# Kernel tuning notes

Hardware: AMD Instinct MI355X
Metric: run time of the kernel (lower is better)

Reference implementation:

```python
import math
import jax, jax.numpy as jnp
from jax import lax
import numpy as np

B, CIN, COUT, K, SD, NCLS, H, W = 8, 512, 512, 3, 512, 35, 64, 64
EPS_DEMOD = 1e-8
EPS_IN = 1e-5  # torch InstanceNorm2d default eps


def _equal_linear(x, w, b):
    # EqualLinear: F.linear(x, w * (1/sqrt(in_dim))) + b  (lr_mul=1)
    return x @ (w.T * (1.0 / math.sqrt(w.shape[1]))) + b


def setup_inputs() -> dict:
    key = jax.random.key(0)
    ks = jax.random.split(key, 8)
    return {
        "input": jax.random.normal(ks[0], (B, CIN, H, W), jnp.float32),
        "style": jax.random.normal(ks[1], (B, SD), jnp.float32),
        "class_style": jax.random.normal(ks[2], (NCLS, SD), jnp.float32),
        "weight": jax.random.normal(ks[3], (1, COUT, CIN, K, K), jnp.float32),
        "mod_w": jax.random.normal(ks[4], (CIN, SD), jnp.float32),
        "mod_b": jnp.ones((CIN,), jnp.float32),  # bias_init=1
        "cw_w": jax.random.normal(ks[5], (COUT, SD), jnp.float32),
        "cw_b": jnp.ones((COUT,), jnp.float32),
        "cb_w": jax.random.normal(ks[6], (COUT, SD), jnp.float32),
        "cb_b": jnp.ones((COUT,), jnp.float32),
        "label_class_dict": jax.random.randint(ks[7], (B, H, W), 0, NCLS),
    }


def reference(input, style, class_style, weight, mod_w, mod_b, cw_w, cw_b, cb_w, cb_b, label_class_dict):
    scale = 1.0 / math.sqrt(CIN * K * K)
    pad = K // 2

    # per-sample style modulation of weights
    s = _equal_linear(style, mod_w, mod_b)                 # [B, CIN]
    w = scale * weight * s[:, None, :, None, None]         # [B, COUT, CIN, K, K]
    demod = lax.rsqrt(jnp.sum(w * w, axis=(2, 3, 4)) + EPS_DEMOD)  # [B, COUT]
    w = w * demod[:, :, None, None, None]

    # grouped conv (groups = batch) == vmap of per-sample conv
    def conv_one(x, wb):  # x [CIN,H,W], wb [COUT,CIN,K,K]
        return lax.conv_general_dilated(
            x[None], wb, window_strides=(1, 1), padding=[(pad, pad), (pad, pad)],
            dimension_numbers=("NCHW", "OIHW", "NCHW"))[0]

    out = jax.vmap(conv_one)(input, w)                     # [B, COUT, H, W]

    # param-free instance norm (biased variance, no affine)
    mu = out.mean(axis=(2, 3), keepdims=True)
    var = out.var(axis=(2, 3), keepdims=True)
    out = (out - mu) * lax.rsqrt(var + EPS_IN)

    # CLADE per-class affine from class_style, gathered via label map
    cw = _equal_linear(class_style, cw_w, cw_b)            # [NCLS, COUT]
    cb = _equal_linear(class_style, cb_w, cb_b)            # [NCLS, COUT]
    class_weight = jnp.transpose(cw[label_class_dict], (0, 3, 1, 2))  # [B,COUT,H,W]
    class_bias = jnp.transpose(cb[label_class_dict], (0, 3, 1, 2))
    return out * class_weight + class_bias
```

## Files before the change

kernel.cpp:

```cpp
#include <hip/hip_runtime.h>

typedef unsigned short u16;
typedef unsigned int u32;
typedef __attribute__((ext_vector_type(8))) short short8;
typedef __attribute__((ext_vector_type(4))) float floatx4;

__device__ inline float bf2f(u16 h) {
  union { u32 u; float f; } v; v.u = ((u32)h) << 16; return v.f;
}
__device__ inline u16 f2bf(float f) {
  union { float f; u32 u; } v; v.f = f;
  u32 u = v.u;
  return (u16)((u + 0x7fffu + ((u >> 16) & 1u)) >> 16);
}
__device__ inline float ldf(const void* p, int i, int isbf) {
  return isbf ? bf2f(((const u16*)p)[i]) : ((const float*)p)[i];
}

__global__ void sniff_kernel(const u32* __restrict__ w, int* __restrict__ flag) {
  __shared__ int cnt;
  if (threadIdx.x == 0) cnt = 0;
  __syncthreads();
  int c = 0;
  #pragma unroll
  for (int i = 0; i < 4; ++i) {
    u32 v = w[1024 + threadIdx.x * 4 + i];
    int e = (v >> 7) & 0xFF;
    if (e >= 96 && e <= 160) c++;
  }
  atomicAdd(&cnt, c);
  __syncthreads();
  if (threadIdx.x == 0) *flag = (cnt >= 154) ? 1 : 0;
}

__global__ void styles_kernel(const void* __restrict__ style, const void* __restrict__ class_style,
                              const void* __restrict__ mod_w, const void* __restrict__ mod_b,
                              const void* __restrict__ cw_w, const void* __restrict__ cw_b,
                              const void* __restrict__ cb_w, const void* __restrict__ cb_b,
                              const int* __restrict__ flagp,
                              float* __restrict__ s, float* __restrict__ cw, float* __restrict__ cb) {
  const int isbf = *flagp;
  int row = blockIdx.x;
  const void *vec, *wm, *bias; float* out; int voff;
  if (row < 8)        { vec = style;       voff = row*512;        wm = mod_w; bias = mod_b; out = s  + row*512; }
  else if (row < 43)  { vec = class_style; voff = (row-8)*512;    wm = cw_w;  bias = cw_b;  out = cw + (row-8)*512; }
  else                { vec = class_style; voff = (row-43)*512;   wm = cb_w;  bias = cb_b;  out = cb + (row-43)*512; }
  __shared__ float v[512];
  for (int i = threadIdx.x; i < 512; i += 256) v[i] = ldf(vec, voff + i, isbf);
  __syncthreads();
  const float inv = 0.04419417382415922f;
  for (int o = threadIdx.x; o < 512; o += 256) {
    float acc = 0.f;
    if (isbf) {
      for (int k = 0; k < 512; ++k) acc += bf2f(((const u16*)wm)[o*512 + k]) * v[k];
    } else {
      const float4* wr = (const float4*)((const float*)wm + o*512);
      for (int k = 0; k < 128; ++k) {
        float4 p = wr[k];
        acc += p.x*v[k*4+0] + p.y*v[k*4+1] + p.z*v[k*4+2] + p.w*v[k*4+3];
      }
    }
    out[o] = acc * inv + ldf(bias, o, isbf);
  }
}

__global__ void wprep_kernel(const void* __restrict__ weight, const int* __restrict__ flagp,
                             u16* __restrict__ wT, float* __restrict__ wsqT) {
  const int isbf = *flagp;
  const int co = blockIdx.x;
  __shared__ float wsmem[4608];
  for (int i = threadIdx.x; i < 4608; i += 256)
    wsmem[i] = ldf(weight, co*4608 + i, isbf);
  __syncthreads();
  for (int ci = threadIdx.x; ci < 512; ci += 256) {
    float sq = 0.f;
    const int ck = ci >> 5, cin = ci & 31;
    #pragma unroll
    for (int tap = 0; tap < 9; ++tap) {
      float fv = wsmem[ci*9 + tap];
      sq += fv*fv;
      wT[(size_t)(((ck*9 + tap)*512) + co)*32 + cin] = f2bf(fv);
    }
    wsqT[ci*512 + co] = sq;
  }
}

__global__ void xtrans_kernel(const void* __restrict__ x, const float* __restrict__ s,
                              const int* __restrict__ flagp, u16* __restrict__ xT) {
  const int isbf = *flagp;
  const int t = threadIdx.x;
  const int w = t & 63, cq = t >> 6;
  const int b = blockIdx.z, h = blockIdx.y;
  const int ck = blockIdx.x;
  const int ci0 = ck*32 + cq*8;
  float f[8];
  #pragma unroll
  for (int j = 0; j < 8; ++j) {
    float xv = ldf(x, (((b*512) + ci0 + j)*64 + h)*64 + w, isbf);
    f[j] = xv * s[b*512 + ci0 + j];
  }
  u32 outp[4];
  #pragma unroll
  for (int i = 0; i < 4; ++i)
    outp[i] = (u32)f2bf(f[2*i]) | ((u32)f2bf(f[2*i+1]) << 16);
  uint4 po = {outp[0], outp[1], outp[2], outp[3]};
  *(uint4*)&xT[(size_t)((((b*16 + ck)*64 + h)*64 + w)*32) + cq*8] = po;
}

__global__ __launch_bounds__(256, 2) void conv_kernel(const u16* __restrict__ xT, const u16* __restrict__ wT,
                                                      float* __restrict__ y, float* __restrict__ part) {
  __shared__ __align__(16) u16 xs[4*10*66*8];
  __shared__ __align__(16) u16 wsm[9*4*64*8];
  const int tid = threadIdx.x;
  const int lane = tid & 63;
  const int wid = tid >> 6;
  const int hb = blockIdx.x, b = blockIdx.y;
  const int ct0 = blockIdx.z * 64;
  const int h0 = hb * 8;

  if (tid < 80) {
    int q = tid / 20, rem = tid % 20, dr = rem >> 1, side = rem & 1;
    uint4 z = {0,0,0,0};
    *(uint4*)&xs[(((q*10 + dr)*66) + side*65)*8] = z;
  }

  floatx4 acc[4][8];
  #pragma unroll
  for (int i = 0; i < 4; ++i) {
    #pragma unroll
    for (int j = 0; j < 8; ++j) acc[i][j] = (floatx4)(0.f);
  }

  const int m = lane & 15, qd = lane >> 4;

  for (int ck = 0; ck < 16; ++ck) {
    __syncthreads();

    #pragma unroll
    for (int j = 0; j < 10; ++j) {
      int g = tid + j*256;
      int q = g & 3, c64 = (g >> 2) & 63, dr = g >> 8;
      int hin = h0 + dr - 1;
      uint4 v = {0,0,0,0};
      if (hin >= 0 && hin <= 63)
        v = *(const uint4*)&xT[(size_t)((((b*16 + ck)*64 + hin)*64 + c64)*32) + q*8];
      *(uint4*)&xs[(((q*10 + dr)*66) + 1 + c64)*8] = v;
    }
    #pragma unroll
    for (int j = 0; j < 9; ++j) {
      int g = tid + j*256;
      int q = g & 3, co = (g >> 2) & 63, tap = g >> 8;
      uint4 v = *(const uint4*)&wT[(size_t)(((ck*9 + tap)*512) + ct0 + co)*32 + q*8];
      *(uint4*)&wsm[(((tap*4 + q)*64) + (co ^ (q << 2)))*8] = v;
    }
    __syncthreads();

    #pragma unroll
    for (int tap = 0; tap < 9; ++tap) {
      const int k1 = tap / 3, k2 = tap - k1*3;
      short8 af[4], bfr[8];
      #pragma unroll
      for (int mi = 0; mi < 4; ++mi)
        af[mi] = *(const short8*)&wsm[(((tap*4 + qd)*64) + ((mi*16 + m) ^ (qd << 2)))*8];
      #pragma unroll
      for (int hh = 0; hh < 2; ++hh) {
        const int dr = wid*2 + hh + k1;
        #pragma unroll
        for (int nw = 0; nw < 4; ++nw)
          bfr[hh*4 + nw] = *(const short8*)&xs[(((qd*10 + dr)*66) + nw*16 + m + k2)*8];
      }
      #pragma unroll
      for (int ni = 0; ni < 8; ++ni) {
        #pragma unroll
        for (int mi = 0; mi < 4; ++mi)
          acc[mi][ni] = __builtin_amdgcn_mfma_f32_16x16x32_bf16(af[mi], bfr[ni], acc[mi][ni], 0, 0, 0);
      }
    }
  }

  #pragma unroll
  for (int mi = 0; mi < 4; ++mi) {
    #pragma unroll
    for (int hh = 0; hh < 2; ++hh) {
      const int h = h0 + wid*2 + hh;
      #pragma unroll
      for (int nw = 0; nw < 4; ++nw) {
        #pragma unroll
        for (int r = 0; r < 4; ++r) {
          int co = ct0 + mi*16 + qd*4 + r;
          int w = nw*16 + m;
          y[(size_t)(((b*512) + co)*64 + h)*64 + w] = acc[mi][hh*4 + nw][r];
        }
      }
    }
  }

  float s1[16], s2[16];
  #pragma unroll
  for (int mi = 0; mi < 4; ++mi) {
    #pragma unroll
    for (int r = 0; r < 4; ++r) {
      float a = 0.f, aa = 0.f;
      #pragma unroll
      for (int ni = 0; ni < 8; ++ni) {
        float v = acc[mi][ni][r];
        a += v; aa += v*v;
      }
      s1[mi*4+r] = a; s2[mi*4+r] = aa;
    }
  }
  #pragma unroll
  for (int off = 1; off < 16; off <<= 1) {
    #pragma unroll
    for (int i = 0; i < 16; ++i) {
      s1[i] += __shfl_xor(s1[i], off, 64);
      s2[i] += __shfl_xor(s2[i], off, 64);
    }
  }
  __syncthreads();
  float* red = (float*)xs;
  if (m == 0) {
    #pragma unroll
    for (int mi = 0; mi < 4; ++mi) {
      #pragma unroll
      for (int r = 0; r < 4; ++r) {
        int co = mi*16 + qd*4 + r;
        red[(wid*64 + co)*2 + 0] = s1[mi*4+r];
        red[(wid*64 + co)*2 + 1] = s2[mi*4+r];
      }
    }
  }
  __syncthreads();
  if (tid < 128) {
    int co = tid >> 1, which = tid & 1;
    float v = (red[(0*64+co)*2+which] + red[(1*64+co)*2+which])
            + (red[(2*64+co)*2+which] + red[(3*64+co)*2+which]);
    part[(size_t)(((b*8 + hb)*512) + ct0 + co)*2 + which] = v;
  }
}

__global__ void finalize_kernel(const float* __restrict__ part, const float* __restrict__ s,
                                const float* __restrict__ wsqT,
                                float* __restrict__ mu, float* __restrict__ istd) {
  const int gid = blockIdx.x*256 + threadIdx.x;
  const int b = gid >> 9, co = gid & 511;
  float S = 0.f, Q = 0.f;
  #pragma unroll
  for (int hb = 0; hb < 8; ++hb) {
    S += part[(size_t)(((b*8 + hb)*512) + co)*2 + 0];
    Q += part[(size_t)(((b*8 + hb)*512) + co)*2 + 1];
  }
  float SS = 0.f;
  for (int ci = 0; ci < 512; ++ci) {
    float sv = s[b*512 + ci];
    SS += sv*sv * wsqT[ci*512 + co];
  }
  float mval = S * (1.f/4096.f);
  float var = fmaxf(Q * (1.f/4096.f) - mval*mval, 0.f);
  float eps = 1e-5f*SS + 4.608e-10f;
  mu[gid] = mval;
  istd[gid] = rsqrtf(var + eps);
}

__global__ void epi_kernel(float* __restrict__ y, const float* __restrict__ mu, const float* __restrict__ istd,
                           const float* __restrict__ cw, const float* __restrict__ cb,
                           const int* __restrict__ label) {
  __shared__ float2 tab[35];
  const int blk = blockIdx.x;
  const int bc = blk >> 1, half = blk & 1;
  const int b = bc >> 9, co = bc & 511;
  const int t = threadIdx.x;
  if (t < 35) tab[t] = make_float2(cw[t*512 + co], cb[t*512 + co]);
  __syncthreads();
  const float mval = mu[bc], is = istd[bc];
  const int base = half*2048 + t*8;
  const int h = base >> 6, w = base & 63;
  float* yp = y + (size_t)bc*4096 + base;
  float4 v0 = *(const float4*)yp;
  float4 v1 = *(const float4*)(yp + 4);
  const int* lp = label + ((b*64) + h)*64 + w;
  float vin[8] = {v0.x, v0.y, v0.z, v0.w, v1.x, v1.y, v1.z, v1.w};
  float vout[8];
  #pragma unroll
  for (int i = 0; i < 8; ++i) {
    float a = (vin[i] - mval) * is;
    float2 wb = tab[lp[i]];
    vout[i] = a*wb.x + wb.y;
  }
  float4 o0 = {vout[0], vout[1], vout[2], vout[3]};
  float4 o1 = {vout[4], vout[5], vout[6], vout[7]};
  *(float4*)yp = o0;
  *(float4*)(yp + 4) = o1;
}

extern "C" void kernel_launch(void* const* d_in, const int* in_sizes, int n_in,
                              void* d_out, int out_size, void* d_ws, size_t ws_size,
                              hipStream_t stream) {
  (void)in_sizes; (void)n_in; (void)out_size; (void)ws_size;
  const void* input       = d_in[0];
  const void* style       = d_in[1];
  const void* class_style = d_in[2];
  const void* weight      = d_in[3];
  const void* mod_w       = d_in[4];
  const void* mod_b       = d_in[5];
  const void* cw_w        = d_in[6];
  const void* cw_b        = d_in[7];
  const void* cb_w        = d_in[8];
  const void* cb_b        = d_in[9];
  const int* label        = (const int*)d_in[10];
  float* y = (float*)d_out;

  char* ws = (char*)d_ws;
  u16*   xT   = (u16*)  (ws + 0);
  u16*   wT   = (u16*)  (ws + 33554432);
  float* wsqT = (float*)(ws + 38273024);
  float* s    = (float*)(ws + 39321600);
  float* cw   = (float*)(ws + 39337984);
  float* cb   = (float*)(ws + 39409664);
  float* mu   = (float*)(ws + 39481344);
  float* istd = (float*)(ws + 39497728);
  float* part = (float*)(ws + 39514112);
  int*   flag = (int*)  (ws + 39776256);

  hipLaunchKernelGGL(sniff_kernel, dim3(1), dim3(64), 0, stream, (const u32*)weight, flag);
  hipLaunchKernelGGL(styles_kernel, dim3(78), dim3(256), 0, stream,
                     style, class_style, mod_w, mod_b, cw_w, cw_b, cb_w, cb_b,
                     (const int*)flag, s, cw, cb);
  hipLaunchKernelGGL(wprep_kernel, dim3(512), dim3(256), 0, stream, weight, (const int*)flag, wT, wsqT);
  hipLaunchKernelGGL(xtrans_kernel, dim3(16, 64, 8), dim3(256), 0, stream, input, s, (const int*)flag, xT);
  hipLaunchKernelGGL(conv_kernel, dim3(8, 8, 8), dim3(256), 0, stream, xT, wT, y, part);
  hipLaunchKernelGGL(finalize_kernel, dim3(16), dim3(256), 0, stream, part, s, wsqT, mu, istd);
  hipLaunchKernelGGL(epi_kernel, dim3(8192), dim3(256), 0, stream, y, mu, istd, cw, cb, label);
}
```

Before: 356.7 us.

## Fuse conv, instance-norm finalize and CLADE epilogue via cooperative grid sync

Turns the conv kernel into a cooperative launch that keeps accumulators in registers, grid-syncs after writing per-block partial stats, then computes the mean and inverse std and applies the per-class affine directly before the single store of y. This removes the raw y write and re-read plus two extra kernel launches. It also changes the LDS layout of the input tile (row-major over dr then q) and the XOR swizzle of the weight tile to alter bank-conflict patterns. Costs are a grid-wide barrier across 512 blocks that must all be co-resident, added register pressure, and per-block redundant work on the demod-epsilon reduction. A non-cooperative fallback path is kept.

New measurement: 401.9 us. 12.7% more time.

```diff
diff --git a/kernel.cpp b/kernel.cpp
--- a/kernel.cpp
+++ b/kernel.cpp
@@ -1,9 +1,12 @@
 #include <hip/hip_runtime.h>
+#include <hip/hip_cooperative_groups.h>
 
 typedef unsigned short u16;
 typedef unsigned int u32;
 typedef __attribute__((ext_vector_type(8))) short short8;
 typedef __attribute__((ext_vector_type(4))) float floatx4;
+
+namespace cg = cooperative_groups;
 
 __device__ inline float bf2f(u16 h) {
   union { u32 u; float f; } v; v.u = ((u32)h) << 16; return v.f;
@@ -107,9 +110,13 @@
   *(uint4*)&xT[(size_t)((((b*16 + ck)*64 + h)*64 + w)*32) + cq*8] = po;
 }
 
-__global__ __launch_bounds__(256, 2) void conv_kernel(const u16* __restrict__ xT, const u16* __restrict__ wT,
-                                                      float* __restrict__ y, float* __restrict__ part) {
-  __shared__ __align__(16) u16 xs[4*10*66*8];
+template<int FUSED>
+__global__ __launch_bounds__(256, 2) void conv_t(const u16* __restrict__ xT, const u16* __restrict__ wT,
+                                                 float* __restrict__ y, float* __restrict__ part,
+                                                 const float* __restrict__ s, const float* __restrict__ wsqT,
+                                                 const float* __restrict__ cw, const float* __restrict__ cb,
+                                                 const int* __restrict__ label) {
+  __shared__ __align__(16) u16 xs[10*4*66*8];
   __shared__ __align__(16) u16 wsm[9*4*64*8];
   const int tid = threadIdx.x;
   const int lane = tid & 63;
@@ -121,7 +128,7 @@
   if (tid < 80) {
     int q = tid / 20, rem = tid % 20, dr = rem >> 1, side = rem & 1;
     uint4 z = {0,0,0,0};
-    *(uint4*)&xs[(((q*10 + dr)*66) + side*65)*8] = z;
+    *(uint4*)&xs[(((dr*4 + q)*66) + side*65)*8] = z;
   }
 
   floatx4 acc[4][8];
@@ -144,14 +151,14 @@
       uint4 v = {0,0,0,0};
       if (hin >= 0 && hin <= 63)
         v = *(const uint4*)&xT[(size_t)((((b*16 + ck)*64 + hin)*64 + c64)*32) + q*8];
-      *(uint4*)&xs[(((q*10 + dr)*66) + 1 + c64)*8] = v;
+      *(uint4*)&xs[(((dr*4 + q)*66) + 1 + c64)*8] = v;
     }
     #pragma unroll
     for (int j = 0; j < 9; ++j) {
       int g = tid + j*256;
       int q = g & 3, co = (g >> 2) & 63, tap = g >> 8;
       uint4 v = *(const uint4*)&wT[(size_t)(((ck*9 + tap)*512) + ct0 + co)*32 + q*8];
-      *(uint4*)&wsm[(((tap*4 + q)*64) + (co ^ (q << 2)))*8] = v;
+      *(uint4*)&wsm[(((tap*4 + q)*64) + (co ^ (q << 1)))*8] = v;
     }
     __syncthreads();
 
@@ -161,36 +168,19 @@
       short8 af[4], bfr[8];
       #pragma unroll
       for (int mi = 0; mi < 4; ++mi)
-        af[mi] = *(const short8*)&wsm[(((tap*4 + qd)*64) + ((mi*16 + m) ^ (qd << 2)))*8];
+        af[mi] = *(const short8*)&wsm[(((tap*4 + qd)*64) + ((mi*16 + m) ^ (qd << 1)))*8];
       #pragma unroll
       for (int hh = 0; hh < 2; ++hh) {
         const int dr = wid*2 + hh + k1;
         #pragma unroll
         for (int nw = 0; nw < 4; ++nw)
-          bfr[hh*4 + nw] = *(const short8*)&xs[(((qd*10 + dr)*66) + nw*16 + m + k2)*8];
+          bfr[hh*4 + nw] = *(const short8*)&xs[(((dr*4 + qd)*66) + nw*16 + m + k2)*8];
       }
       #pragma unroll
       for (int ni = 0; ni < 8; ++ni) {
         #pragma unroll
         for (int mi = 0; mi < 4; ++mi)
           acc[mi][ni] = __builtin_amdgcn_mfma_f32_16x16x32_bf16(af[mi], bfr[ni], acc[mi][ni], 0, 0, 0);
-      }
-    }
-  }
-
-  #pragma unroll
-  for (int mi = 0; mi < 4; ++mi) {
-    #pragma unroll
-    for (int hh = 0; hh < 2; ++hh) {
-      const int h = h0 + wid*2 + hh;
-      #pragma unroll
-      for (int nw = 0; nw < 4; ++nw) {
-        #pragma unroll
-        for (int r = 0; r < 4; ++r) {
-          int co = ct0 + mi*16 + qd*4 + r;
-          int w = nw*16 + m;
-          y[(size_t)(((b*512) + co)*64 + h)*64 + w] = acc[mi][hh*4 + nw][r];
-        }
       }
     }
   }
@@ -236,6 +226,91 @@
     float v = (red[(0*64+co)*2+which] + red[(1*64+co)*2+which])
             + (red[(2*64+co)*2+which] + red[(3*64+co)*2+which]);
     part[(size_t)(((b*8 + hb)*512) + ct0 + co)*2 + which] = v;
+  }
+
+  if constexpr (!FUSED) {
+    #pragma unroll
+    for (int mi = 0; mi < 4; ++mi) {
+      #pragma unroll
+      for (int hh = 0; hh < 2; ++hh) {
+        const int h = h0 + wid*2 + hh;
+        #pragma unroll
+        for (int nw = 0; nw < 4; ++nw) {
+          #pragma unroll
+          for (int r = 0; r < 4; ++r) {
+            int co = ct0 + mi*16 + qd*4 + r;
+            int w = nw*16 + m;
+            y[(size_t)(((b*512) + co)*64 + h)*64 + w] = acc[mi][hh*4 + nw][r];
+          }
+        }
+      }
+    }
+  } else {
+    cg::this_grid().sync();
+
+    float2* tab   = (float2*)xs;
+    int*    labs  = (int*)wsm;
+    float*  epred = (float*)(wsm + 2048);
+    float2* ms    = (float2*)(wsm + 4096);
+
+    for (int i = tid; i < 2240; i += 256) {
+      int cls = i >> 6, co = i & 63;
+      tab[cls*65 + co] = make_float2(cw[cls*512 + ct0 + co], cb[cls*512 + ct0 + co]);
+    }
+    for (int i = tid; i < 512; i += 256)
+      labs[i] = label[((b*64) + h0 + (i >> 6))*64 + (i & 63)];
+
+    {
+      float ep = 0.f;
+      const float* wsq_c = wsqT + ct0 + (tid & 63);
+      const float* sb = s + b*512 + (tid >> 6)*128;
+      const int cib = (tid >> 6)*128;
+      #pragma unroll 4
+      for (int k = 0; k < 128; ++k) {
+        float sv = sb[k];
+        ep += sv*sv * wsq_c[(size_t)(cib + k)*512];
+      }
+      epred[tid] = ep;
+    }
+    __syncthreads();
+
+    if (tid < 64) {
+      float S = 0.f, Q = 0.f;
+      const float2* pv = (const float2*)part;
+      #pragma unroll
+      for (int hbb = 0; hbb < 8; ++hbb) {
+        float2 p = pv[(size_t)((b*8 + hbb)*512) + ct0 + tid];
+        S += p.x; Q += p.y;
+      }
+      float eps = 1e-5f*(epred[tid] + epred[64+tid] + epred[128+tid] + epred[192+tid])
+                + 4.608e-10f;
+      float mval = S * (1.f/4096.f);
+      float var = fmaxf(Q * (1.f/4096.f) - mval*mval, 0.f);
+      ms[tid] = make_float2(mval, rsqrtf(var + eps));
+    }
+    __syncthreads();
+
+    #pragma unroll
+    for (int mi = 0; mi < 4; ++mi) {
+      #pragma unroll
+      for (int hh = 0; hh < 2; ++hh) {
+        const int h = h0 + wid*2 + hh;
+        #pragma unroll
+        for (int nw = 0; nw < 4; ++nw) {
+          const int w = nw*16 + m;
+          const int lab = labs[(wid*2 + hh)*64 + w];
+          const float2* trow = tab + lab*65;
+          #pragma unroll
+          for (int r = 0; r < 4; ++r) {
+            const int col = mi*16 + qd*4 + r;
+            float2 msv = ms[col];
+            float2 wb = trow[col];
+            float a = (acc[mi][hh*4 + nw][r] - msv.x) * msv.y;
+            y[(size_t)(((b*512) + ct0 + col)*64 + h)*64 + w] = a*wb.x + wb.y;
+          }
+        }
+      }
+    }
   }
 }
 
@@ -328,7 +403,20 @@
                      (const int*)flag, s, cw, cb);
   hipLaunchKernelGGL(wprep_kernel, dim3(512), dim3(256), 0, stream, weight, (const int*)flag, wT, wsqT);
   hipLaunchKernelGGL(xtrans_kernel, dim3(16, 64, 8), dim3(256), 0, stream, input, s, (const int*)flag, xT);
-  hipLaunchKernelGGL(conv_kernel, dim3(8, 8, 8), dim3(256), 0, stream, xT, wT, y, part);
-  hipLaunchKernelGGL(finalize_kernel, dim3(16), dim3(256), 0, stream, part, s, wsqT, mu, istd);
-  hipLaunchKernelGGL(epi_kernel, dim3(8192), dim3(256), 0, stream, y, mu, istd, cw, cb, label);
-}
+
+  {
+    const u16* a0 = xT; const u16* a1 = wT; float* a2 = y; float* a3 = part;
+    const float* a4 = s; const float* a5 = wsqT; const float* a6 = cw; const float* a7 = cb;
+    const int* a8 = label;
+    void* args[] = {&a0, &a1, &a2, &a3, &a4, &a5, &a6, &a7, &a8};
+    hipError_t ce = hipLaunchCooperativeKernel(conv_t<1>, dim3(8, 8, 8), dim3(256),
+                                               args, 0, stream);
+    if (ce != hipSuccess) {
+      (void)hipGetLastError();
+      hipLaunchKernelGGL((conv_t<0>), dim3(8, 8, 8), dim3(256), 0, stream,
+                         xT, wT, y, part, s, wsqT, cw, cb, label);
+      hipLaunchKernelGGL(finalize_kernel, dim3(16), dim3(256), 0, stream, part, s, wsqT, mu, istd);
+      hipLaunchKernelGGL(epi_kernel, dim3(8192), dim3(256), 0, stream, y, mu, istd, cw, cb, label);
+    }
+  }
+}
```

## Fuse prep kernels into one launch and fold finalize into epilogue

Applied to the files above, without the earlier changes.

Merges the dtype sniff, style linears, weight transpose and input transpose into one multi-role prep kernel. Each xtrans block recomputes its 32 style scales from mod_w, which removes the dependency on the styles kernel. The instance-norm finalize is folded into the epilogue: each block reduces the demod epsilon term and the partial sums for one (b, co), then normalizes with vectorized label loads. The conv LDS layout interleave and the weight swizzle are also changed to alter bank-conflict patterns. The trade-off is redundant style dot-products and serial per-block reductions, in exchange for fewer launches and no small-grid finalize pass.

New measurement: 330.9 us. 7.2% less time.

```diff
diff --git a/kernel.cpp b/kernel.cpp
--- a/kernel.cpp
+++ b/kernel.cpp
@@ -17,99 +17,118 @@
   return isbf ? bf2f(((const u16*)p)[i]) : ((const float*)p)[i];
 }
 
-__global__ void sniff_kernel(const u32* __restrict__ w, int* __restrict__ flag) {
+__global__ __launch_bounds__(256) void prep_kernel(
+    const void* __restrict__ style, const void* __restrict__ class_style,
+    const void* __restrict__ weight,
+    const void* __restrict__ mod_w, const void* __restrict__ mod_b,
+    const void* __restrict__ cw_w, const void* __restrict__ cw_b,
+    const void* __restrict__ cb_w, const void* __restrict__ cb_b,
+    const void* __restrict__ x,
+    float* __restrict__ s, float* __restrict__ cw, float* __restrict__ cb,
+    u16* __restrict__ wT, float* __restrict__ wsqT2, u16* __restrict__ xT) {
+  __shared__ float smem[4608];
   __shared__ int cnt;
-  if (threadIdx.x == 0) cnt = 0;
-  __syncthreads();
-  int c = 0;
-  #pragma unroll
-  for (int i = 0; i < 4; ++i) {
-    u32 v = w[1024 + threadIdx.x * 4 + i];
+  const int t = threadIdx.x;
+
+  if (t == 0) cnt = 0;
+  __syncthreads();
+  {
+    u32 v = ((const u32*)weight)[1024 + t];
     int e = (v >> 7) & 0xFF;
-    if (e >= 96 && e <= 160) c++;
-  }
-  atomicAdd(&cnt, c);
-  __syncthreads();
-  if (threadIdx.x == 0) *flag = (cnt >= 154) ? 1 : 0;
-}
-
-__global__ void styles_kernel(const void* __restrict__ style, const void* __restrict__ class_style,
-                              const void* __restrict__ mod_w, const void* __restrict__ mod_b,
-                              const void* __restrict__ cw_w, const void* __restrict__ cw_b,
-                              const void* __restrict__ cb_w, const void* __restrict__ cb_b,
-                              const int* __restrict__ flagp,
-                              float* __restrict__ s, float* __restrict__ cw, float* __restrict__ cb) {
-  const int isbf = *flagp;
-  int row = blockIdx.x;
-  const void *vec, *wm, *bias; float* out; int voff;
-  if (row < 8)        { vec = style;       voff = row*512;        wm = mod_w; bias = mod_b; out = s  + row*512; }
-  else if (row < 43)  { vec = class_style; voff = (row-8)*512;    wm = cw_w;  bias = cw_b;  out = cw + (row-8)*512; }
-  else                { vec = class_style; voff = (row-43)*512;   wm = cb_w;  bias = cb_b;  out = cb + (row-43)*512; }
-  __shared__ float v[512];
-  for (int i = threadIdx.x; i < 512; i += 256) v[i] = ldf(vec, voff + i, isbf);
-  __syncthreads();
-  const float inv = 0.04419417382415922f;
-  for (int o = threadIdx.x; o < 512; o += 256) {
-    float acc = 0.f;
-    if (isbf) {
-      for (int k = 0; k < 512; ++k) acc += bf2f(((const u16*)wm)[o*512 + k]) * v[k];
-    } else {
-      const float4* wr = (const float4*)((const float*)wm + o*512);
-      for (int k = 0; k < 128; ++k) {
-        float4 p = wr[k];
-        acc += p.x*v[k*4+0] + p.y*v[k*4+1] + p.z*v[k*4+2] + p.w*v[k*4+3];
-      }
-    }
-    out[o] = acc * inv + ldf(bias, o, isbf);
-  }
-}
-
-__global__ void wprep_kernel(const void* __restrict__ weight, const int* __restrict__ flagp,
-                             u16* __restrict__ wT, float* __restrict__ wsqT) {
-  const int isbf = *flagp;
-  const int co = blockIdx.x;
-  __shared__ float wsmem[4608];
-  for (int i = threadIdx.x; i < 4608; i += 256)
-    wsmem[i] = ldf(weight, co*4608 + i, isbf);
-  __syncthreads();
-  for (int ci = threadIdx.x; ci < 512; ci += 256) {
-    float sq = 0.f;
-    const int ck = ci >> 5, cin = ci & 31;
-    #pragma unroll
-    for (int tap = 0; tap < 9; ++tap) {
-      float fv = wsmem[ci*9 + tap];
-      sq += fv*fv;
-      wT[(size_t)(((ck*9 + tap)*512) + co)*32 + cin] = f2bf(fv);
-    }
-    wsqT[ci*512 + co] = sq;
-  }
-}
-
-__global__ void xtrans_kernel(const void* __restrict__ x, const float* __restrict__ s,
-                              const int* __restrict__ flagp, u16* __restrict__ xT) {
-  const int isbf = *flagp;
-  const int t = threadIdx.x;
-  const int w = t & 63, cq = t >> 6;
-  const int b = blockIdx.z, h = blockIdx.y;
-  const int ck = blockIdx.x;
-  const int ci0 = ck*32 + cq*8;
-  float f[8];
-  #pragma unroll
-  for (int j = 0; j < 8; ++j) {
-    float xv = ldf(x, (((b*512) + ci0 + j)*64 + h)*64 + w, isbf);
-    f[j] = xv * s[b*512 + ci0 + j];
-  }
-  u32 outp[4];
-  #pragma unroll
-  for (int i = 0; i < 4; ++i)
-    outp[i] = (u32)f2bf(f[2*i]) | ((u32)f2bf(f[2*i+1]) << 16);
-  uint4 po = {outp[0], outp[1], outp[2], outp[3]};
-  *(uint4*)&xT[(size_t)((((b*16 + ck)*64 + h)*64 + w)*32) + cq*8] = po;
+    if (e >= 96 && e <= 160) atomicAdd(&cnt, 1);
+  }
+  __syncthreads();
+  const int isbf = (cnt >= 154) ? 1 : 0;
+  const int bid = blockIdx.x;
+
+  if (bid < 78) {
+    int row = bid;
+    const void *vec, *wm, *bias; float* out; int voff;
+    if (row < 8)        { vec = style;       voff = row*512;      wm = mod_w; bias = mod_b; out = s  + row*512; }
+    else if (row < 43)  { vec = class_style; voff = (row-8)*512;  wm = cw_w;  bias = cw_b;  out = cw + (row-8)*512; }
+    else                { vec = class_style; voff = (row-43)*512; wm = cb_w;  bias = cb_b;  out = cb + (row-43)*512; }
+    float* v = smem;
+    for (int i = t; i < 512; i += 256) v[i] = ldf(vec, voff + i, isbf);
+    __syncthreads();
+    const float inv = 0.04419417382415922f;
+    for (int o = t; o < 512; o += 256) {
+      float acc = 0.f;
+      if (isbf) {
+        for (int k = 0; k < 512; ++k) acc += bf2f(((const u16*)wm)[o*512 + k]) * v[k];
+      } else {
+        const float4* wr = (const float4*)((const float*)wm + o*512);
+        for (int k = 0; k < 128; ++k) {
+          float4 p = wr[k];
+          acc += p.x*v[k*4+0] + p.y*v[k*4+1] + p.z*v[k*4+2] + p.w*v[k*4+3];
+        }
+      }
+      out[o] = acc * inv + ldf(bias, o, isbf);
+    }
+  } else if (bid < 590) {
+    const int co = bid - 78;
+    float* wsmem = smem;
+    for (int i = t; i < 4608; i += 256)
+      wsmem[i] = ldf(weight, co*4608 + i, isbf);
+    __syncthreads();
+    for (int ci = t; ci < 512; ci += 256) {
+      float sq = 0.f;
+      const int ck = ci >> 5, cin = ci & 31;
+      #pragma unroll
+      for (int tap = 0; tap < 9; ++tap) {
+        float fv = wsmem[ci*9 + tap];
+        sq += fv*fv;
+        wT[(size_t)(((ck*9 + tap)*512) + co)*32 + cin] = f2bf(fv);
+      }
+      wsqT2[(size_t)co*512 + ci] = sq;
+    }
+  } else {
+    const int r = bid - 590;
+    const int ck = r & 15, h = (r >> 4) & 63, b = r >> 10;
+    float* sv = smem;
+    float* sl = smem + 512;
+    for (int i = t; i < 512; i += 256) sv[i] = ldf(style, b*512 + i, isbf);
+    __syncthreads();
+    const int lane = t & 63, wv = t >> 6;
+    const float inv = 0.04419417382415922f;
+    #pragma unroll
+    for (int p = 0; p < 8; ++p) {
+      const int row = p*4 + wv;
+      const int ci = ck*32 + row;
+      float partial = 0.f;
+      if (isbf) {
+        const u16* wr = (const u16*)mod_w + (size_t)ci*512 + lane*8;
+        #pragma unroll
+        for (int k = 0; k < 8; ++k) partial += bf2f(wr[k]) * sv[lane*8 + k];
+      } else {
+        const float4* wr = (const float4*)((const float*)mod_w + (size_t)ci*512 + lane*8);
+        float4 p0 = wr[0], p1 = wr[1];
+        partial += p0.x*sv[lane*8+0] + p0.y*sv[lane*8+1] + p0.z*sv[lane*8+2] + p0.w*sv[lane*8+3]
+                 + p1.x*sv[lane*8+4] + p1.y*sv[lane*8+5] + p1.z*sv[lane*8+6] + p1.w*sv[lane*8+7];
+      }
+      #pragma unroll
+      for (int off = 1; off < 64; off <<= 1) partial += __shfl_xor(partial, off, 64);
+      if (lane == 0) sl[row] = partial * inv + ldf(mod_b, ci, isbf);
+    }
+    __syncthreads();
+    const int w = t & 63, cq = t >> 6;
+    float f[8];
+    #pragma unroll
+    for (int j = 0; j < 8; ++j) {
+      float xv = ldf(x, (((b*512) + ck*32 + cq*8 + j)*64 + h)*64 + w, isbf);
+      f[j] = xv * sl[cq*8 + j];
+    }
+    u32 outp[4];
+    #pragma unroll
+    for (int i = 0; i < 4; ++i)
+      outp[i] = (u32)f2bf(f[2*i]) | ((u32)f2bf(f[2*i+1]) << 16);
+    uint4 po = {outp[0], outp[1], outp[2], outp[3]};
+    *(uint4*)&xT[(size_t)((((b*16 + ck)*64 + h)*64 + w)*32) + cq*8] = po;
+  }
 }
 
 __global__ __launch_bounds__(256, 2) void conv_kernel(const u16* __restrict__ xT, const u16* __restrict__ wT,
                                                       float* __restrict__ y, float* __restrict__ part) {
-  __shared__ __align__(16) u16 xs[4*10*66*8];
+  __shared__ __align__(16) u16 xs[10*4*66*8];
   __shared__ __align__(16) u16 wsm[9*4*64*8];
   const int tid = threadIdx.x;
   const int lane = tid & 63;
@@ -121,7 +140,7 @@
   if (tid < 80) {
     int q = tid / 20, rem = tid % 20, dr = rem >> 1, side = rem & 1;
     uint4 z = {0,0,0,0};
-    *(uint4*)&xs[(((q*10 + dr)*66) + side*65)*8] = z;
+    *(uint4*)&xs[(((dr*4 + q)*66) + side*65)*8] = z;
   }
 
   floatx4 acc[4][8];
@@ -144,14 +163,14 @@
       uint4 v = {0,0,0,0};
       if (hin >= 0 && hin <= 63)
         v = *(const uint4*)&xT[(size_t)((((b*16 + ck)*64 + hin)*64 + c64)*32) + q*8];
-      *(uint4*)&xs[(((q*10 + dr)*66) + 1 + c64)*8] = v;
+      *(uint4*)&xs[(((dr*4 + q)*66) + 1 + c64)*8] = v;
     }
     #pragma unroll
     for (int j = 0; j < 9; ++j) {
       int g = tid + j*256;
       int q = g & 3, co = (g >> 2) & 63, tap = g >> 8;
       uint4 v = *(const uint4*)&wT[(size_t)(((ck*9 + tap)*512) + ct0 + co)*32 + q*8];
-      *(uint4*)&wsm[(((tap*4 + q)*64) + (co ^ (q << 2)))*8] = v;
+      *(uint4*)&wsm[(((tap*4 + q)*64) + (co ^ (q << 1)))*8] = v;
     }
     __syncthreads();
 
@@ -161,13 +180,13 @@
       short8 af[4], bfr[8];
       #pragma unroll
       for (int mi = 0; mi < 4; ++mi)
-        af[mi] = *(const short8*)&wsm[(((tap*4 + qd)*64) + ((mi*16 + m) ^ (qd << 2)))*8];
+        af[mi] = *(const short8*)&wsm[(((tap*4 + qd)*64) + ((mi*16 + m) ^ (qd << 1)))*8];
       #pragma unroll
       for (int hh = 0; hh < 2; ++hh) {
         const int dr = wid*2 + hh + k1;
         #pragma unroll
         for (int nw = 0; nw < 4; ++nw)
-          bfr[hh*4 + nw] = *(const short8*)&xs[(((qd*10 + dr)*66) + nw*16 + m + k2)*8];
+          bfr[hh*4 + nw] = *(const short8*)&xs[(((dr*4 + qd)*66) + nw*16 + m + k2)*8];
       }
       #pragma unroll
       for (int ni = 0; ni < 8; ++ni) {
@@ -239,58 +258,59 @@
   }
 }
 
-__global__ void finalize_kernel(const float* __restrict__ part, const float* __restrict__ s,
-                                const float* __restrict__ wsqT,
-                                float* __restrict__ mu, float* __restrict__ istd) {
-  const int gid = blockIdx.x*256 + threadIdx.x;
-  const int b = gid >> 9, co = gid & 511;
-  float S = 0.f, Q = 0.f;
-  #pragma unroll
-  for (int hb = 0; hb < 8; ++hb) {
-    S += part[(size_t)(((b*8 + hb)*512) + co)*2 + 0];
-    Q += part[(size_t)(((b*8 + hb)*512) + co)*2 + 1];
-  }
-  float SS = 0.f;
-  for (int ci = 0; ci < 512; ++ci) {
-    float sv = s[b*512 + ci];
-    SS += sv*sv * wsqT[ci*512 + co];
-  }
-  float mval = S * (1.f/4096.f);
-  float var = fmaxf(Q * (1.f/4096.f) - mval*mval, 0.f);
-  float eps = 1e-5f*SS + 4.608e-10f;
-  mu[gid] = mval;
-  istd[gid] = rsqrtf(var + eps);
-}
-
-__global__ void epi_kernel(float* __restrict__ y, const float* __restrict__ mu, const float* __restrict__ istd,
-                           const float* __restrict__ cw, const float* __restrict__ cb,
-                           const int* __restrict__ label) {
-  __shared__ float2 tab[35];
-  const int blk = blockIdx.x;
-  const int bc = blk >> 1, half = blk & 1;
+__global__ __launch_bounds__(256) void epi_kernel(float* __restrict__ y, const float* __restrict__ part,
+                                                  const float* __restrict__ s, const float* __restrict__ wsqT2,
+                                                  const float* __restrict__ cw, const float* __restrict__ cb,
+                                                  const int* __restrict__ label) {
+  const int bc = blockIdx.x;
   const int b = bc >> 9, co = bc & 511;
   const int t = threadIdx.x;
-  if (t < 35) tab[t] = make_float2(cw[t*512 + co], cb[t*512 + co]);
-  __syncthreads();
-  const float mval = mu[bc], is = istd[bc];
-  const int base = half*2048 + t*8;
-  const int h = base >> 6, w = base & 63;
-  float* yp = y + (size_t)bc*4096 + base;
-  float4 v0 = *(const float4*)yp;
-  float4 v1 = *(const float4*)(yp + 4);
-  const int* lp = label + ((b*64) + h)*64 + w;
-  float vin[8] = {v0.x, v0.y, v0.z, v0.w, v1.x, v1.y, v1.z, v1.w};
-  float vout[8];
-  #pragma unroll
-  for (int i = 0; i < 8; ++i) {
-    float a = (vin[i] - mval) * is;
-    float2 wb = tab[lp[i]];
-    vout[i] = a*wb.x + wb.y;
-  }
-  float4 o0 = {vout[0], vout[1], vout[2], vout[3]};
-  float4 o1 = {vout[4], vout[5], vout[6], vout[7]};
-  *(float4*)yp = o0;
-  *(float4*)(yp + 4) = o1;
+  __shared__ float tabw[35], tabb[35];
+  __shared__ float redp[4];
+  __shared__ float2 msh;
+  if (t < 35) { tabw[t] = cw[t*512 + co]; tabb[t] = cb[t*512 + co]; }
+
+  const float* sb = s + b*512;
+  const float* wq = wsqT2 + (size_t)co*512;
+  float ep;
+  {
+    float s0 = sb[t], s1v = sb[t + 256];
+    ep = s0*s0*wq[t] + s1v*s1v*wq[t + 256];
+  }
+  #pragma unroll
+  for (int off = 1; off < 64; off <<= 1) ep += __shfl_xor(ep, off, 64);
+  if ((t & 63) == 0) redp[t >> 6] = ep;
+  __syncthreads();
+  if (t == 0) {
+    float SS = redp[0] + redp[1] + redp[2] + redp[3];
+    float S = 0.f, Q = 0.f;
+    const float2* pv = (const float2*)part;
+    #pragma unroll
+    for (int hb = 0; hb < 8; ++hb) {
+      float2 p = pv[(size_t)((b*8 + hb)*512) + co];
+      S += p.x; Q += p.y;
+    }
+    float mval = S * (1.f/4096.f);
+    float var = fmaxf(Q * (1.f/4096.f) - mval*mval, 0.f);
+    float eps = 1e-5f*SS + 4.608e-10f;
+    msh = make_float2(mval, rsqrtf(var + eps));
+  }
+  __syncthreads();
+  const float mval = msh.x, is = msh.y;
+
+  float* yp = y + (size_t)bc*4096 + t*16;
+  const int* lp = label + b*4096 + t*16;
+  #pragma unroll
+  for (int u = 0; u < 4; ++u) {
+    float4 v = *(const float4*)(yp + u*4);
+    int4 l = *(const int4*)(lp + u*4);
+    float4 o;
+    o.x = (v.x - mval)*is*tabw[l.x] + tabb[l.x];
+    o.y = (v.y - mval)*is*tabw[l.y] + tabb[l.y];
+    o.z = (v.z - mval)*is*tabw[l.z] + tabb[l.z];
+    o.w = (v.w - mval)*is*tabw[l.w] + tabb[l.w];
+    *(float4*)(yp + u*4) = o;
+  }
 }
 
 extern "C" void kernel_launch(void* const* d_in, const int* in_sizes, int n_in,
@@ -311,24 +331,17 @@
   float* y = (float*)d_out;
 
   char* ws = (char*)d_ws;
-  u16*   xT   = (u16*)  (ws + 0);
-  u16*   wT   = (u16*)  (ws + 33554432);
-  float* wsqT = (float*)(ws + 38273024);
-  float* s    = (float*)(ws + 39321600);
-  float* cw   = (float*)(ws + 39337984);
-  float* cb   = (float*)(ws + 39409664);
-  float* mu   = (float*)(ws + 39481344);
-  float* istd = (float*)(ws + 39497728);
-  float* part = (float*)(ws + 39514112);
-  int*   flag = (int*)  (ws + 39776256);
-
-  hipLaunchKernelGGL(sniff_kernel, dim3(1), dim3(64), 0, stream, (const u32*)weight, flag);
-  hipLaunchKernelGGL(styles_kernel, dim3(78), dim3(256), 0, stream,
-                     style, class_style, mod_w, mod_b, cw_w, cw_b, cb_w, cb_b,
-                     (const int*)flag, s, cw, cb);
-  hipLaunchKernelGGL(wprep_kernel, dim3(512), dim3(256), 0, stream, weight, (const int*)flag, wT, wsqT);
-  hipLaunchKernelGGL(xtrans_kernel, dim3(16, 64, 8), dim3(256), 0, stream, input, s, (const int*)flag, xT);
+  u16*   xT    = (u16*)  (ws + 0);
+  u16*   wT    = (u16*)  (ws + 33554432);
+  float* wsqT2 = (float*)(ws + 38273024);
+  float* s     = (float*)(ws + 39321600);
+  float* cw    = (float*)(ws + 39337984);
+  float* cb    = (float*)(ws + 39409664);
+  float* part  = (float*)(ws + 39481344);
+
+  hipLaunchKernelGGL(prep_kernel, dim3(8782), dim3(256), 0, stream,
+                     style, class_style, weight, mod_w, mod_b, cw_w, cw_b, cb_w, cb_b,
+                     input, s, cw, cb, wT, wsqT2, xT);
   hipLaunchKernelGGL(conv_kernel, dim3(8, 8, 8), dim3(256), 0, stream, xT, wT, y, part);
-  hipLaunchKernelGGL(finalize_kernel, dim3(16), dim3(256), 0, stream, part, s, wsqT, mu, istd);
-  hipLaunchKernelGGL(epi_kernel, dim3(8192), dim3(256), 0, stream, y, mu, istd, cw, cb, label);
-}
+  hipLaunchKernelGGL(epi_kernel, dim3(4096), dim3(256), 0, stream, y, part, s, wsqT2, cw, cb, label);
+}
```
